# Kernel tuning notes

Measured on AMD Instinct MI355X. Metric: run time of the kernel, lower is better.

## Reference

```python
import jax, jax.numpy as jnp
import numpy as np

GROUP = 128               # group_size
SCALE = float(np.sqrt(GROUP))  # self._scale = sqrt(group_size)
M, N, T = 4096, 4096, 512  # out_features, in_features, tokens


def _rotation(seed: int, n: int) -> jnp.ndarray:
    """Seeded random orthogonal rotation via QR (rotation='qr')."""
    g = np.random.default_rng(seed)
    q, _ = np.linalg.qr(g.standard_normal((n, n)))
    return jnp.asarray(q.astype(np.float32))


def setup_inputs() -> dict:
    key = jax.random.key(0)
    ks = jax.random.split(key, 7)
    x = jax.random.normal(ks[0], (T, N), jnp.float32)
    Pi = _rotation(42, N)    # pass-1 rotation seed (default _rotation_seed = 42)
    Pi2 = _rotation(43, N)   # pass-2 rotation seed
    indices_packed = jax.random.randint(ks[1], (M, N // 2), 0, 256, jnp.int32)
    weight_norms = jax.random.uniform(ks[2], (M, N // GROUP), jnp.float32, 0.5, 1.5)
    codebook = jnp.sort(jax.random.normal(ks[3], (16,), jnp.float32))  # Lloyd-Max centroids
    pass2_indices_packed = jax.random.randint(ks[4], (M, N // 2), 0, 256, jnp.int32)
    pass2_weight_norms = jax.random.uniform(ks[5], (M, N // GROUP), jnp.float32, 0.05, 0.15)
    pass2_codebook = jnp.sort(jax.random.normal(ks[6], (16,), jnp.float32)) * 0.1
    return {
        'x': x, 'Pi': Pi,
        'indices_packed': indices_packed, 'weight_norms': weight_norms, 'codebook': codebook,
        'pass2_indices_packed': pass2_indices_packed, 'pass2_weight_norms': pass2_weight_norms,
        'pass2_codebook': pass2_codebook, 'Pi2': Pi2,
    }


def _dequant(indices_packed, weight_norms, codebook):
    """Unpack 4-bit indices, gather centroids, apply per-group norm scaling.

    indices_packed: (M, N//2) int (uint8 values), low nibble = even column.
    Returns dequantized weight W of shape (M, N).
    """
    low = indices_packed & 0xF
    high = (indices_packed >> 4) & 0xF
    idx = jnp.stack([low, high], axis=-1).reshape(indices_packed.shape[0], -1)  # (M, N)
    w = codebook[idx]                                        # (M, N) centroid gather
    scale = jnp.repeat(weight_norms * (1.0 / SCALE), GROUP, axis=1)  # (M, N)
    return w * scale


def reference(x, Pi, indices_packed, weight_norms, codebook,
              pass2_indices_packed, pass2_weight_norms, pass2_codebook, Pi2):
    # Pass 1: rotate input, multiply by dequantized weight
    W1 = _dequant(indices_packed, weight_norms, codebook)       # (M, N)
    out = (x @ Pi.T) @ W1.T                                     # (T, M)
    # Pass 2 (residual): independent rotation + dequantized residual weight
    W2 = _dequant(pass2_indices_packed, pass2_weight_norms, pass2_codebook)
    out = out + (x @ Pi2.T) @ W2.T
    return out
```

## Files before the change

### kernel.cpp

```cpp
#include <hip/hip_runtime.h>
#include <hip/hip_bf16.h>


typedef __bf16 bf16x8 __attribute__((ext_vector_type(8)));
typedef float  f32x4  __attribute__((ext_vector_type(4)));

#define T_DIM   512
#define N_DIM   4096
#define M_DIM   4096
#define K2_DIM  8192
#define INV_SQRT_G 0.08838834764831843f

typedef const __attribute__((address_space(1))) unsigned int as1_u32;
typedef __attribute__((address_space(3)))       unsigned int as3_u32;

__device__ __forceinline__ void gload16(const void* g, void* l) {
    __builtin_amdgcn_global_load_lds((as1_u32*)g, (as3_u32*)l, 16, 0, 0);
}

__global__ __launch_bounds__(256) void cvt_x_kernel(
    const float* __restrict__ x, __bf16* __restrict__ xb)
{
    int i = (blockIdx.x * 256 + threadIdx.x) * 8;
    float4 f0 = *(const float4*)&x[i];
    float4 f1 = *(const float4*)&x[i + 4];
    bf16x8 h = { (__bf16)f0.x, (__bf16)f0.y, (__bf16)f0.z, (__bf16)f0.w,
                 (__bf16)f1.x, (__bf16)f1.y, (__bf16)f1.z, (__bf16)f1.w };
    *(bf16x8*)&xb[i] = h;
}

__global__ __launch_bounds__(256, 2) void gemm1_kernel(
    const __bf16* __restrict__ xb, const float* __restrict__ Pi,
    const float* __restrict__ Pi2, __bf16* __restrict__ Y)
{
    __shared__ __bf16 sA[2][128 * 64];
    __shared__ __bf16 sB[2][64 * 64];

    const int tid = threadIdx.x;
    const int n0  = blockIdx.x * 64;
    const int t0  = blockIdx.y * 128;
    const float* Bsrc = (n0 < N_DIM) ? Pi : Pi2;
    const int nloc = n0 & (N_DIM - 1);

    const int wid = tid >> 6, lane = tid & 63;
    const int wr = (wid >> 1) * 64, wc = (wid & 1) * 32;
    const int lr = lane & 15, lg = lane >> 4;

    const int arow = wid * 8 + (lane >> 3);
    const int acol = (lane & 7) * 8;
    const int sr = tid >> 2, sc = (tid & 3) * 16;

    f32x4 acc[4][2] = {};
    float4 rb[4];

    auto issueA = [&](int buf, int k0) {
        #pragma unroll
        for (int c = 0; c < 4; ++c)
            gload16(&xb[(size_t)(t0 + c * 32 + arow) * N_DIM + k0 + acol],
                    &sA[buf][c * 2048 + wid * 512]);
    };
    auto loadB = [&](int k0) {
        const float* bp = &Bsrc[(size_t)(nloc + sr) * N_DIM + k0 + sc];
        #pragma unroll
        for (int q = 0; q < 4; ++q) rb[q] = *(const float4*)(bp + q * 4);
    };
    auto writeB = [&](int buf) {
        #pragma unroll
        for (int h = 0; h < 2; ++h) {
            float4 f0 = rb[h * 2], f1 = rb[h * 2 + 1];
            bf16x8 v = { (__bf16)f0.x, (__bf16)f0.y, (__bf16)f0.z, (__bf16)f0.w,
                         (__bf16)f1.x, (__bf16)f1.y, (__bf16)f1.z, (__bf16)f1.w };
            *(bf16x8*)&sB[buf][sr * 64 + sc + h * 8] = v;
        }
    };

    loadB(0);
    issueA(0, 0);
    writeB(0);
    __syncthreads();

    int cur = 0;
    for (int k = 0; k < N_DIM / 64; ++k) {
        const int k0n = (k + 1) * 64;
        if (k0n < N_DIM) { loadB(k0n); issueA(cur ^ 1, k0n); }

        bf16x8 af[4][2], bfr[2][2];
        #pragma unroll
        for (int m = 0; m < 4; ++m)
            #pragma unroll
            for (int kh = 0; kh < 2; ++kh)
                af[m][kh] = *(const bf16x8*)&sA[cur][(wr + m * 16 + lr) * 64 + kh * 32 + lg * 8];
        #pragma unroll
        for (int n = 0; n < 2; ++n)
            #pragma unroll
            for (int kh = 0; kh < 2; ++kh)
                bfr[n][kh] = *(const bf16x8*)&sB[cur][(wc + n * 16 + lr) * 64 + kh * 32 + lg * 8];
        #pragma unroll
        for (int m = 0; m < 4; ++m)
            #pragma unroll
            for (int n = 0; n < 2; ++n)
                #pragma unroll
                for (int kh = 0; kh < 2; ++kh)
                    acc[m][n] = __builtin_amdgcn_mfma_f32_16x16x32_bf16(
                        af[m][kh], bfr[n][kh], acc[m][n], 0, 0, 0);

        if (k0n < N_DIM) writeB(cur ^ 1);
        __syncthreads();
        cur ^= 1;
    }

    #pragma unroll
    for (int m = 0; m < 4; ++m)
        #pragma unroll
        for (int n = 0; n < 2; ++n)
            #pragma unroll
            for (int e = 0; e < 4; ++e)
                Y[(size_t)(t0 + wr + m * 16 + lg * 4 + e) * K2_DIM +
                  n0 + wc + n * 16 + lr] = (__bf16)acc[m][n][e];
}

__global__ __launch_bounds__(256, 2) void gemm2_kernel(
    const __bf16* __restrict__ Y,
    const int*   __restrict__ idx1, const float* __restrict__ wn1,
    const float* __restrict__ cb1,
    const int*   __restrict__ idx2, const float* __restrict__ wn2,
    const float* __restrict__ cb2,
    float* __restrict__ out)
{
    __shared__ __bf16 sA[2][128 * 64];
    __shared__ __bf16 sB[2][64 * 64];
    __shared__ float2 lut[256];

    const int tid  = threadIdx.x;
    const int m0   = blockIdx.x * 64;
    const int t0   = blockIdx.y * 128;
    const int pass = blockIdx.z;

    const int*   idxp = pass ? idx2 : idx1;
    const float* wn   = pass ? wn2  : wn1;
    const float* cbg  = pass ? cb2  : cb1;

    {
        float lo = cbg[tid & 15] * INV_SQRT_G;
        float hi = cbg[(tid >> 4) & 15] * INV_SQRT_G;
        lut[tid] = make_float2(lo, hi);
    }

    const int wid = tid >> 6, lane = tid & 63;
    const int wr = (wid >> 1) * 64, wc = (wid & 1) * 32;
    const int lr = lane & 15, lg = lane >> 4;

    const int arow = wid * 8 + (lane >> 3);
    const int acol = (lane & 7) * 8;
    const int sr = tid >> 2, s4 = tid & 3;

    f32x4 acc[4][2] = {};
    int4  wi[2];
    float wscale;

    auto issueA = [&](int buf, int kl) {
        #pragma unroll
        for (int c = 0; c < 4; ++c)
            gload16(&Y[(size_t)(t0 + c * 32 + arow) * K2_DIM + pass * N_DIM + kl + acol],
                    &sA[buf][c * 2048 + wid * 512]);
    };
    auto loadB = [&](int kl) {
        const int* ip = &idxp[(size_t)(m0 + sr) * (N_DIM / 2) + (kl >> 1) + s4 * 8];
        wi[0] = *(const int4*)ip;
        wi[1] = *(const int4*)(ip + 4);
        wscale = wn[(size_t)(m0 + sr) * 32 + (kl >> 7)];
    };
    auto writeB = [&](int buf) {
        #pragma unroll
        for (int h = 0; h < 2; ++h) {
            int4 v = wi[h];
            float2 p0 = lut[v.x & 255], p1 = lut[v.y & 255];
            float2 p2 = lut[v.z & 255], p3 = lut[v.w & 255];
            bf16x8 w = { (__bf16)(p0.x * wscale), (__bf16)(p0.y * wscale),
                         (__bf16)(p1.x * wscale), (__bf16)(p1.y * wscale),
                         (__bf16)(p2.x * wscale), (__bf16)(p2.y * wscale),
                         (__bf16)(p3.x * wscale), (__bf16)(p3.y * wscale) };
            *(bf16x8*)&sB[buf][sr * 64 + s4 * 16 + h * 8] = w;
        }
    };

    loadB(0);
    issueA(0, 0);
    __syncthreads();
    writeB(0);
    __syncthreads();

    int cur = 0;
    for (int k = 0; k < N_DIM / 64; ++k) {
        const int kln = (k + 1) * 64;
        if (kln < N_DIM) { loadB(kln); issueA(cur ^ 1, kln); }

        bf16x8 af[4][2], bfr[2][2];
        #pragma unroll
        for (int m = 0; m < 4; ++m)
            #pragma unroll
            for (int kh = 0; kh < 2; ++kh)
                af[m][kh] = *(const bf16x8*)&sA[cur][(wr + m * 16 + lr) * 64 + kh * 32 + lg * 8];
        #pragma unroll
        for (int n = 0; n < 2; ++n)
            #pragma unroll
            for (int kh = 0; kh < 2; ++kh)
                bfr[n][kh] = *(const bf16x8*)&sB[cur][(wc + n * 16 + lr) * 64 + kh * 32 + lg * 8];
        #pragma unroll
        for (int m = 0; m < 4; ++m)
            #pragma unroll
            for (int n = 0; n < 2; ++n)
                #pragma unroll
                for (int kh = 0; kh < 2; ++kh)
                    acc[m][n] = __builtin_amdgcn_mfma_f32_16x16x32_bf16(
                        af[m][kh], bfr[n][kh], acc[m][n], 0, 0, 0);

        if (kln < N_DIM) writeB(cur ^ 1);
        __syncthreads();
        cur ^= 1;
    }

    #pragma unroll
    for (int m = 0; m < 4; ++m)
        #pragma unroll
        for (int n = 0; n < 2; ++n)
            #pragma unroll
            for (int e = 0; e < 4; ++e)
                atomicAdd(&out[(size_t)(t0 + wr + m * 16 + lg * 4 + e) * M_DIM +
                               m0 + wc + n * 16 + lr], acc[m][n][e]);
}

extern "C" void kernel_launch(void* const* d_in, const int* in_sizes, int n_in,
                              void* d_out, int out_size, void* d_ws, size_t ws_size,
                              hipStream_t stream) {
    const float* x    = (const float*)d_in[0];
    const float* Pi   = (const float*)d_in[1];
    const int*   idx1 = (const int*)  d_in[2];
    const float* wn1  = (const float*)d_in[3];
    const float* cb1  = (const float*)d_in[4];
    const int*   idx2 = (const int*)  d_in[5];
    const float* wn2  = (const float*)d_in[6];
    const float* cb2  = (const float*)d_in[7];
    const float* Pi2  = (const float*)d_in[8];
    float* out = (float*)d_out;

    __bf16* xb = (__bf16*)d_ws;
    __bf16* Yw = (__bf16*)((char*)d_ws + (size_t)T_DIM * N_DIM * sizeof(__bf16));

    hipMemsetAsync(d_out, 0, (size_t)T_DIM * M_DIM * sizeof(float), stream);

    cvt_x_kernel<<<dim3(T_DIM * N_DIM / (256 * 8)), dim3(256), 0, stream>>>(x, xb);
    gemm1_kernel<<<dim3(K2_DIM / 64, T_DIM / 128), dim3(256), 0, stream>>>(xb, Pi, Pi2, Yw);
    gemm2_kernel<<<dim3(M_DIM / 64, T_DIM / 128, 2), dim3(256), 0, stream>>>(
        Yw, idx1, wn1, cb1, idx2, wn2, cb2, out);
}
```

Before: 386.8 us.

## Use 128x128 tiles with K=32 steps, swizzled LDS, and split-K for both GEMMs

Both GEMMs move from 128x64 to 128x128 output tiles with a 32-wide K step and an XOR-swizzled B layout in shared memory, raising the occupancy hint to 3. GEMM2 splits K four ways and accumulates with unsafeAtomicAdd. GEMM1 can also split K four ways into an fp32 scratch buffer followed by a bf16 conversion pass when workspace allows. The aim is more blocks in flight to fill the GPU plus more MFMA work per LDS load. The cost is extra atomic traffic, an extra memset and conversion pass, and nondeterministic summation order.

```diff
diff --git a/kernel.cpp b/kernel.cpp
--- a/kernel.cpp
+++ b/kernel.cpp
@@ -29,38 +29,55 @@
     *(bf16x8*)&xb[i] = h;
 }
 
-__global__ __launch_bounds__(256, 2) void gemm1_kernel(
+__global__ __launch_bounds__(256) void cvt_y_kernel(
+    const float* __restrict__ Y32, __bf16* __restrict__ Y)
+{
+    int i = (blockIdx.x * 256 + threadIdx.x) * 8;
+    float4 f0 = *(const float4*)&Y32[i];
+    float4 f1 = *(const float4*)&Y32[i + 4];
+    bf16x8 h = { (__bf16)f0.x, (__bf16)f0.y, (__bf16)f0.z, (__bf16)f0.w,
+                 (__bf16)f1.x, (__bf16)f1.y, (__bf16)f1.z, (__bf16)f1.w };
+    *(bf16x8*)&Y[i] = h;
+}
+
+template<bool SPLITK>
+__global__ __launch_bounds__(256, 3) void gemm1_kernel(
     const __bf16* __restrict__ xb, const float* __restrict__ Pi,
-    const float* __restrict__ Pi2, __bf16* __restrict__ Y)
-{
-    __shared__ __bf16 sA[2][128 * 64];
-    __shared__ __bf16 sB[2][64 * 64];
-
-    const int tid = threadIdx.x;
-    const int n0  = blockIdx.x * 64;
-    const int t0  = blockIdx.y * 128;
+    const float* __restrict__ Pi2, float* __restrict__ Y32,
+    __bf16* __restrict__ Y)
+{
+    __shared__ __bf16 sA[2][128 * 32];
+    __shared__ __bf16 sB[2][128 * 32];
+
+    const int tid   = threadIdx.x;
+    const int n0    = blockIdx.x * 128;
+    const int t0    = blockIdx.y * 128;
+    const int kbase = blockIdx.z * (SPLITK ? 1024 : N_DIM);
+    const int NK    = (SPLITK ? 1024 : N_DIM) / 32;
+
     const float* Bsrc = (n0 < N_DIM) ? Pi : Pi2;
     const int nloc = n0 & (N_DIM - 1);
 
     const int wid = tid >> 6, lane = tid & 63;
-    const int wr = (wid >> 1) * 64, wc = (wid & 1) * 32;
+    const int wr = (wid >> 1) * 64, wc = (wid & 1) * 64;
     const int lr = lane & 15, lg = lane >> 4;
-
-    const int arow = wid * 8 + (lane >> 3);
-    const int acol = (lane & 7) * 8;
-    const int sr = tid >> 2, sc = (tid & 3) * 16;
-
-    f32x4 acc[4][2] = {};
+    const int sw = lr & 3;
+
+    const int arow = wid * 16 + (lane >> 2);
+    const int acol = (lane & 3) * 8;
+    const int br = tid >> 1, bh = tid & 1;
+
+    f32x4 acc[4][4] = {};
     float4 rb[4];
 
     auto issueA = [&](int buf, int k0) {
         #pragma unroll
-        for (int c = 0; c < 4; ++c)
-            gload16(&xb[(size_t)(t0 + c * 32 + arow) * N_DIM + k0 + acol],
-                    &sA[buf][c * 2048 + wid * 512]);
+        for (int c = 0; c < 2; ++c)
+            gload16(&xb[(size_t)(t0 + c * 64 + arow) * N_DIM + k0 + acol],
+                    &sA[buf][(c * 64 + wid * 16) * 32]);
     };
     auto loadB = [&](int k0) {
-        const float* bp = &Bsrc[(size_t)(nloc + sr) * N_DIM + k0 + sc];
+        const float* bp = &Bsrc[(size_t)(nloc + br) * N_DIM + k0 + bh * 16];
         #pragma unroll
         for (int q = 0; q < 4; ++q) rb[q] = *(const float4*)(bp + q * 4);
     };
@@ -70,41 +87,36 @@
             float4 f0 = rb[h * 2], f1 = rb[h * 2 + 1];
             bf16x8 v = { (__bf16)f0.x, (__bf16)f0.y, (__bf16)f0.z, (__bf16)f0.w,
                          (__bf16)f1.x, (__bf16)f1.y, (__bf16)f1.z, (__bf16)f1.w };
-            *(bf16x8*)&sB[buf][sr * 64 + sc + h * 8] = v;
+            int unit = (bh * 2 + h) ^ (br & 3);
+            *(bf16x8*)&sB[buf][br * 32 + unit * 8] = v;
         }
     };
 
-    loadB(0);
-    issueA(0, 0);
+    loadB(kbase);
+    issueA(0, kbase);
     writeB(0);
     __syncthreads();
 
     int cur = 0;
-    for (int k = 0; k < N_DIM / 64; ++k) {
-        const int k0n = (k + 1) * 64;
-        if (k0n < N_DIM) { loadB(k0n); issueA(cur ^ 1, k0n); }
-
-        bf16x8 af[4][2], bfr[2][2];
-        #pragma unroll
-        for (int m = 0; m < 4; ++m)
-            #pragma unroll
-            for (int kh = 0; kh < 2; ++kh)
-                af[m][kh] = *(const bf16x8*)&sA[cur][(wr + m * 16 + lr) * 64 + kh * 32 + lg * 8];
-        #pragma unroll
-        for (int n = 0; n < 2; ++n)
-            #pragma unroll
-            for (int kh = 0; kh < 2; ++kh)
-                bfr[n][kh] = *(const bf16x8*)&sB[cur][(wc + n * 16 + lr) * 64 + kh * 32 + lg * 8];
-        #pragma unroll
-        for (int m = 0; m < 4; ++m)
-            #pragma unroll
-            for (int n = 0; n < 2; ++n)
-                #pragma unroll
-                for (int kh = 0; kh < 2; ++kh)
-                    acc[m][n] = __builtin_amdgcn_mfma_f32_16x16x32_bf16(
-                        af[m][kh], bfr[n][kh], acc[m][n], 0, 0, 0);
-
-        if (k0n < N_DIM) writeB(cur ^ 1);
+    for (int k = 0; k < NK; ++k) {
+        const int kn = kbase + (k + 1) * 32;
+        if (k + 1 < NK) { loadB(kn); issueA(cur ^ 1, kn); }
+
+        bf16x8 af[4], bf[4];
+        #pragma unroll
+        for (int m = 0; m < 4; ++m)
+            af[m] = *(const bf16x8*)&sA[cur][(wr + m * 16 + lr) * 32 + lg * 8];
+        #pragma unroll
+        for (int n = 0; n < 4; ++n)
+            bf[n] = *(const bf16x8*)&sB[cur][(wc + n * 16 + lr) * 32 + (lg ^ sw) * 8];
+        #pragma unroll
+        for (int m = 0; m < 4; ++m)
+            #pragma unroll
+            for (int n = 0; n < 4; ++n)
+                acc[m][n] = __builtin_amdgcn_mfma_f32_16x16x32_bf16(
+                    af[m], bf[n], acc[m][n], 0, 0, 0);
+
+        if (k + 1 < NK) writeB(cur ^ 1);
         __syncthreads();
         cur ^= 1;
     }
@@ -112,14 +124,17 @@
     #pragma unroll
     for (int m = 0; m < 4; ++m)
         #pragma unroll
-        for (int n = 0; n < 2; ++n)
-            #pragma unroll
-            for (int e = 0; e < 4; ++e)
-                Y[(size_t)(t0 + wr + m * 16 + lg * 4 + e) * K2_DIM +
-                  n0 + wc + n * 16 + lr] = (__bf16)acc[m][n][e];
-}
-
-__global__ __launch_bounds__(256, 2) void gemm2_kernel(
+        for (int n = 0; n < 4; ++n)
+            #pragma unroll
+            for (int e = 0; e < 4; ++e) {
+                size_t off = (size_t)(t0 + wr + m * 16 + lg * 4 + e) * K2_DIM +
+                             n0 + wc + n * 16 + lr;
+                if (SPLITK) unsafeAtomicAdd(&Y32[off], acc[m][n][e]);
+                else        Y[off] = (__bf16)acc[m][n][e];
+            }
+}
+
+__global__ __launch_bounds__(256, 3) void gemm2_kernel(
     const __bf16* __restrict__ Y,
     const int*   __restrict__ idx1, const float* __restrict__ wn1,
     const float* __restrict__ cb1,
@@ -127,48 +142,47 @@
     const float* __restrict__ cb2,
     float* __restrict__ out)
 {
-    __shared__ __bf16 sA[2][128 * 64];
-    __shared__ __bf16 sB[2][64 * 64];
+    __shared__ __bf16 sA[2][128 * 32];
+    __shared__ __bf16 sB[2][128 * 32];
     __shared__ float2 lut[256];
 
     const int tid  = threadIdx.x;
-    const int m0   = blockIdx.x * 64;
+    const int m0   = blockIdx.x * 128;
     const int t0   = blockIdx.y * 128;
-    const int pass = blockIdx.z;
+    const int pass = blockIdx.z >> 2;
+    const int kof  = (blockIdx.z & 3) * 1024;
 
     const int*   idxp = pass ? idx2 : idx1;
     const float* wn   = pass ? wn2  : wn1;
     const float* cbg  = pass ? cb2  : cb1;
 
-    {
-        float lo = cbg[tid & 15] * INV_SQRT_G;
-        float hi = cbg[(tid >> 4) & 15] * INV_SQRT_G;
-        lut[tid] = make_float2(lo, hi);
-    }
+    lut[tid] = make_float2(cbg[tid & 15] * INV_SQRT_G,
+                           cbg[(tid >> 4) & 15] * INV_SQRT_G);
 
     const int wid = tid >> 6, lane = tid & 63;
-    const int wr = (wid >> 1) * 64, wc = (wid & 1) * 32;
+    const int wr = (wid >> 1) * 64, wc = (wid & 1) * 64;
     const int lr = lane & 15, lg = lane >> 4;
-
-    const int arow = wid * 8 + (lane >> 3);
-    const int acol = (lane & 7) * 8;
-    const int sr = tid >> 2, s4 = tid & 3;
-
-    f32x4 acc[4][2] = {};
+    const int sw = lr & 3;
+
+    const int arow = wid * 16 + (lane >> 2);
+    const int acol = (lane & 3) * 8;
+    const int br = tid >> 1, bh = tid & 1;
+
+    f32x4 acc[4][4] = {};
     int4  wi[2];
     float wscale;
 
     auto issueA = [&](int buf, int kl) {
         #pragma unroll
-        for (int c = 0; c < 4; ++c)
-            gload16(&Y[(size_t)(t0 + c * 32 + arow) * K2_DIM + pass * N_DIM + kl + acol],
-                    &sA[buf][c * 2048 + wid * 512]);
+        for (int c = 0; c < 2; ++c)
+            gload16(&Y[(size_t)(t0 + c * 64 + arow) * K2_DIM + pass * N_DIM + kl + acol],
+                    &sA[buf][(c * 64 + wid * 16) * 32]);
     };
     auto loadB = [&](int kl) {
-        const int* ip = &idxp[(size_t)(m0 + sr) * (N_DIM / 2) + (kl >> 1) + s4 * 8];
+        const int* ip = &idxp[(size_t)(m0 + br) * (N_DIM / 2) + (kl >> 1) + bh * 8];
         wi[0] = *(const int4*)ip;
         wi[1] = *(const int4*)(ip + 4);
-        wscale = wn[(size_t)(m0 + sr) * 32 + (kl >> 7)];
+        wscale = wn[(size_t)(m0 + br) * 32 + (kl >> 7)];
     };
     auto writeB = [&](int buf) {
         #pragma unroll
@@ -180,42 +194,38 @@
                          (__bf16)(p1.x * wscale), (__bf16)(p1.y * wscale),
                          (__bf16)(p2.x * wscale), (__bf16)(p2.y * wscale),
                          (__bf16)(p3.x * wscale), (__bf16)(p3.y * wscale) };
-            *(bf16x8*)&sB[buf][sr * 64 + s4 * 16 + h * 8] = w;
+            int unit = (bh * 2 + h) ^ (br & 3);
+            *(bf16x8*)&sB[buf][br * 32 + unit * 8] = w;
         }
     };
 
-    loadB(0);
-    issueA(0, 0);
+    loadB(kof);
+    issueA(0, kof);
     __syncthreads();
     writeB(0);
     __syncthreads();
 
     int cur = 0;
-    for (int k = 0; k < N_DIM / 64; ++k) {
-        const int kln = (k + 1) * 64;
-        if (kln < N_DIM) { loadB(kln); issueA(cur ^ 1, kln); }
-
-        bf16x8 af[4][2], bfr[2][2];
-        #pragma unroll
-        for (int m = 0; m < 4; ++m)
-            #pragma unroll
-            for (int kh = 0; kh < 2; ++kh)
-                af[m][kh] = *(const bf16x8*)&sA[cur][(wr + m * 16 + lr) * 64 + kh * 32 + lg * 8];
-        #pragma unroll
-        for (int n = 0; n < 2; ++n)
-            #pragma unroll
-            for (int kh = 0; kh < 2; ++kh)
-                bfr[n][kh] = *(const bf16x8*)&sB[cur][(wc + n * 16 + lr) * 64 + kh * 32 + lg * 8];
-        #pragma unroll
-        for (int m = 0; m < 4; ++m)
-            #pragma unroll
-            for (int n = 0; n < 2; ++n)
-                #pragma unroll
-                for (int kh = 0; kh < 2; ++kh)
-                    acc[m][n] = __builtin_amdgcn_mfma_f32_16x16x32_bf16(
-                        af[m][kh], bfr[n][kh], acc[m][n], 0, 0, 0);
-
-        if (kln < N_DIM) writeB(cur ^ 1);
+    const int NK = 1024 / 32;
+    for (int k = 0; k < NK; ++k) {
+        const int kn = kof + (k + 1) * 32;
+        if (k + 1 < NK) { loadB(kn); issueA(cur ^ 1, kn); }
+
+        bf16x8 af[4], bf[4];
+        #pragma unroll
+        for (int m = 0; m < 4; ++m)
+            af[m] = *(const bf16x8*)&sA[cur][(wr + m * 16 + lr) * 32 + lg * 8];
+        #pragma unroll
+        for (int n = 0; n < 4; ++n)
+            bf[n] = *(const bf16x8*)&sB[cur][(wc + n * 16 + lr) * 32 + (lg ^ sw) * 8];
+        #pragma unroll
+        for (int m = 0; m < 4; ++m)
+            #pragma unroll
+            for (int n = 0; n < 4; ++n)
+                acc[m][n] = __builtin_amdgcn_mfma_f32_16x16x32_bf16(
+                    af[m], bf[n], acc[m][n], 0, 0, 0);
+
+        if (k + 1 < NK) writeB(cur ^ 1);
         __syncthreads();
         cur ^= 1;
     }
@@ -223,11 +233,11 @@
     #pragma unroll
     for (int m = 0; m < 4; ++m)
         #pragma unroll
-        for (int n = 0; n < 2; ++n)
+        for (int n = 0; n < 4; ++n)
             #pragma unroll
             for (int e = 0; e < 4; ++e)
-                atomicAdd(&out[(size_t)(t0 + wr + m * 16 + lg * 4 + e) * M_DIM +
-                               m0 + wc + n * 16 + lr], acc[m][n][e]);
+                unsafeAtomicAdd(&out[(size_t)(t0 + wr + m * 16 + lg * 4 + e) * M_DIM +
+                                     m0 + wc + n * 16 + lr], acc[m][n][e]);
 }
 
 extern "C" void kernel_launch(void* const* d_in, const int* in_sizes, int n_in,
@@ -244,13 +254,29 @@
     const float* Pi2  = (const float*)d_in[8];
     float* out = (float*)d_out;
 
-    __bf16* xb = (__bf16*)d_ws;
-    __bf16* Yw = (__bf16*)((char*)d_ws + (size_t)T_DIM * N_DIM * sizeof(__bf16));
-
-    hipMemsetAsync(d_out, 0, (size_t)T_DIM * M_DIM * sizeof(float), stream);
-
+    const size_t xb_bytes  = (size_t)T_DIM * N_DIM * sizeof(__bf16);
+    const size_t y32_bytes = (size_t)T_DIM * K2_DIM * sizeof(float);
+    const size_t y_bytes   = (size_t)T_DIM * K2_DIM * sizeof(__bf16);
+    const bool   splitk    = ws_size >= xb_bytes + y32_bytes + y_bytes;
+
+    __bf16* xb  = (__bf16*)d_ws;
+    float*  Y32 = (float*)((char*)d_ws + xb_bytes);
+    __bf16* Yb  = splitk ? (__bf16*)((char*)d_ws + xb_bytes + y32_bytes)
+                         : (__bf16*)((char*)d_ws + xb_bytes);
+
+    hipMemsetAsync(out, 0, (size_t)T_DIM * M_DIM * sizeof(float), stream);
     cvt_x_kernel<<<dim3(T_DIM * N_DIM / (256 * 8)), dim3(256), 0, stream>>>(x, xb);
-    gemm1_kernel<<<dim3(K2_DIM / 64, T_DIM / 128), dim3(256), 0, stream>>>(xb, Pi, Pi2, Yw);
-    gemm2_kernel<<<dim3(M_DIM / 64, T_DIM / 128, 2), dim3(256), 0, stream>>>(
-        Yw, idx1, wn1, cb1, idx2, wn2, cb2, out);
-}
+
+    if (splitk) {
+        hipMemsetAsync(Y32, 0, y32_bytes, stream);
+        gemm1_kernel<true><<<dim3(K2_DIM / 128, T_DIM / 128, 4), dim3(256), 0, stream>>>(
+            xb, Pi, Pi2, Y32, Yb);
+        cvt_y_kernel<<<dim3(T_DIM * K2_DIM / (256 * 8)), dim3(256), 0, stream>>>(Y32, Yb);
+    } else {
+        gemm1_kernel<false><<<dim3(K2_DIM / 128, T_DIM / 128, 1), dim3(256), 0, stream>>>(
+            xb, Pi, Pi2, Y32, Yb);
+    }
+
+    gemm2_kernel<<<dim3(M_DIM / 128, T_DIM / 128, 8), dim3(256), 0, stream>>>(
+        Yb, idx1, wn1, cb1, idx2, wn2, cb2, out);
+}
```

Result: faster. 379.3 us (-2.0%).
